# Performance work log

Hardware: AMD Instinct MI355X
Metric: run time of the kernel (lower is better)

## Reference

```python
import jax, jax.numpy as jnp
import numpy as np

NUM_HEADS = 16
LN_EPS = 1e-5


def _layer_norm(x, w, b, eps=LN_EPS):
    m = jnp.mean(x, axis=-1, keepdims=True)
    v = jnp.var(x, axis=-1, keepdims=True)
    return (x - m) / jnp.sqrt(v + eps) * w + b


def setup_inputs() -> dict:
    key = jax.random.key(0)
    L, D, DFF, B, S = 16, 1024, 4096, 4, 1024
    ks = jax.random.split(key, 6)
    w_scale = 0.02
    return {
        "x": jax.random.normal(ks[0], (B, S, D), jnp.float32),
        "qkv_w": jax.random.normal(ks[1], (L, 3 * D, D), jnp.float32) * w_scale,
        "qkv_b": jnp.zeros((L, 3 * D), jnp.float32),
        "out_w": jax.random.normal(ks[2], (L, D, D), jnp.float32) * w_scale,
        "out_b": jnp.zeros((L, D), jnp.float32),
        "w1": jax.random.normal(ks[3], (L, DFF, D), jnp.float32) * w_scale,
        "b1": jnp.zeros((L, DFF), jnp.float32),
        "w2": jax.random.normal(ks[4], (L, D, DFF), jnp.float32) * w_scale,
        "b2": jnp.zeros((L, D), jnp.float32),
        "ln1_w": jnp.ones((L, D), jnp.float32),
        "ln1_b": jnp.zeros((L, D), jnp.float32),
        "ln2_w": jnp.ones((L, D), jnp.float32),
        "ln2_b": jnp.zeros((L, D), jnp.float32),
    }


def reference(x, qkv_w, qkv_b, out_w, out_b, w1, b1, w2, b2, ln1_w, ln1_b, ln2_w, ln2_b):
    # T2STransformer.process_prompt: stack of T2SBlocks with causal attention.
    B, S, D = x.shape
    H = NUM_HEADS
    dh = D // H
    # causal additive bias [1,1,S,S]; True on/below diagonal -> attend
    causal = jnp.tril(jnp.ones((S, S), bool))
    bias = jnp.where(causal, 0.0, -jnp.inf).astype(x.dtype)[None, None]
    scale = 1.0 / np.sqrt(dh)

    def step(h, p):
        (qw, qb, ow, ob, mw1, mb1, mw2, mb2, l1w, l1b, l2w, l2b) = p
        qkv = h @ qw.T + qb                      # [B,S,3D]
        q, k, v = jnp.split(qkv, 3, axis=-1)
        q = q.reshape(B, S, H, dh).transpose(0, 2, 1, 3)  # [B,H,S,dh]
        k = k.reshape(B, S, H, dh).transpose(0, 2, 1, 3)
        v = v.reshape(B, S, H, dh).transpose(0, 2, 1, 3)
        scores = jnp.einsum("bhqd,bhkd->bhqk", q, k) * scale + bias
        attn = jax.nn.softmax(scores, axis=-1)
        ctx = jnp.einsum("bhqk,bhkd->bhqd", attn, v)
        ctx = ctx.transpose(0, 2, 1, 3).reshape(B, S, D)
        h = h + (ctx @ ow.T + ob)
        h = _layer_norm(h, l1w, l1b)
        mlp = jax.nn.relu(h @ mw1.T + mb1) @ mw2.T + mb2
        h = _layer_norm(h + mlp, l2w, l2b)
        return h, None

    params = (qkv_w, qkv_b, out_w, out_b, w1, b1, w2, b2, ln1_w, ln1_b, ln2_w, ln2_b)
    out, _ = jax.lax.scan(step, x, params)
    return out
```

## Files before the change

### kernel.cpp

```cpp
#include <hip/hip_runtime.h>
#include <hip/hip_bf16.h>

typedef float f32x4 __attribute__((ext_vector_type(4)));
typedef __bf16 bf16x8 __attribute__((ext_vector_type(8)));
typedef unsigned short ushort_t;

__device__ __forceinline__ unsigned short f2bf(float f) {
    unsigned int u = __builtin_bit_cast(unsigned int, f);
    u += 0x7fffu + ((u >> 16) & 1u);
    return (unsigned short)(u >> 16);
}

#define GCAST(p) ((const __attribute__((address_space(1))) void*)(p))
#define LCAST(p) ((__attribute__((address_space(3))) void*)(p))

__device__ __forceinline__ bf16x8 ldsw(const unsigned short* T, int row, int bcol) {
    return *reinterpret_cast<const bf16x8*>(
        reinterpret_cast<const char*>(T) + row * 128 + (bcol ^ ((row & 7) << 4)));
}

__global__ __launch_bounds__(256) void convert_weights_kernel(
    const float* __restrict__ qw, const float* __restrict__ ow,
    const float* __restrict__ w1, const float* __restrict__ w2,
    unsigned short* __restrict__ dst)
{
    int i = blockIdx.x * 256 + threadIdx.x;
    const float* src; int off;
    if (i < 786432)       { src = qw; off = i; }
    else if (i < 1048576) { src = ow; off = i - 786432; }
    else if (i < 2097152) { src = w1; off = i - 1048576; }
    else                  { src = w2; off = i - 2097152; }
    float4 v = ((const float4*)src)[off];
    ushort4 u;
    u.x = f2bf(v.x); u.y = f2bf(v.y); u.z = f2bf(v.z); u.w = f2bf(v.w);
    ((ushort4*)dst)[i] = u;
}

__global__ __launch_bounds__(256) void gemm_kernel(
    const unsigned short* __restrict__ A, const unsigned short* __restrict__ W,
    const float* __restrict__ bias, void* __restrict__ Cout,
    int N, int K, int relu, int out_bf16)
{
    __shared__ alignas(16) unsigned short As[128][64];
    __shared__ alignas(16) unsigned short Bs[128][64];

    const int tid  = threadIdx.x;
    const int bn   = blockIdx.x, bm = blockIdx.y;
    const int wave = tid >> 6, lane = tid & 63;
    const int wm   = (wave >> 1) * 64, wn = (wave & 1) * 64;
    const int l15  = lane & 15, quad = lane >> 4;
    const int srow = lane >> 3;
    const int scol = (lane & 7) * 8;

    f32x4 acc[4][4];
#pragma unroll
    for (int i = 0; i < 4; i++)
#pragma unroll
        for (int j = 0; j < 4; j++) acc[i][j] = f32x4{0.f, 0.f, 0.f, 0.f};

    const unsigned short* Abase = A + (size_t)(bm * 128) * K;
    const unsigned short* Wbase = W + (size_t)(bn * 128) * K;

    for (int k0 = 0; k0 < K; k0 += 64) {
        __syncthreads();
#pragma unroll
        for (int i = 0; i < 4; i++) {
            int r0 = (i * 4 + wave) * 8;
            __builtin_amdgcn_global_load_lds(
                GCAST(&Abase[(size_t)(r0 + srow) * K + k0 + scol]),
                LCAST(&As[r0][0]), 16, 0, 0);
            __builtin_amdgcn_global_load_lds(
                GCAST(&Wbase[(size_t)(r0 + srow) * K + k0 + scol]),
                LCAST(&Bs[r0][0]), 16, 0, 0);
        }
        __syncthreads();

#pragma unroll
        for (int ks = 0; ks < 2; ks++) {
            bf16x8 a[4], b[4];
#pragma unroll
            for (int mt = 0; mt < 4; mt++)
                a[mt] = *reinterpret_cast<const bf16x8*>(&As[wm + mt * 16 + l15][ks * 32 + quad * 8]);
#pragma unroll
            for (int nt = 0; nt < 4; nt++)
                b[nt] = *reinterpret_cast<const bf16x8*>(&Bs[wn + nt * 16 + l15][ks * 32 + quad * 8]);
#pragma unroll
            for (int mt = 0; mt < 4; mt++)
#pragma unroll
                for (int nt = 0; nt < 4; nt++)
                    acc[mt][nt] = __builtin_amdgcn_mfma_f32_16x16x32_bf16(
                        a[mt], b[nt], acc[mt][nt], 0, 0, 0);
        }
    }

    float* Cf = (float*)Cout;
    unsigned short* Cb = (unsigned short*)Cout;
#pragma unroll
    for (int nt = 0; nt < 4; nt++) {
        int gn = bn * 128 + wn + nt * 16 + l15;
        float bv = bias[gn];
#pragma unroll
        for (int mt = 0; mt < 4; mt++) {
            int gm0 = bm * 128 + wm + mt * 16 + quad * 4;
#pragma unroll
            for (int r = 0; r < 4; r++) {
                float v = acc[mt][nt][r] + bv;
                if (relu) v = fmaxf(v, 0.f);
                if (out_bf16) Cb[(size_t)(gm0 + r) * N + gn] = f2bf(v);
                else          Cf[(size_t)(gm0 + r) * N + gn] = v;
            }
        }
    }
}

__global__ __launch_bounds__(256) void attn_kernel(
    const unsigned short* __restrict__ qkv, unsigned short* __restrict__ ctx)
{
    const int qt = blockIdx.x;
    const int bh = blockIdx.y;
    const int b  = bh >> 4, h = bh & 15;
    const int tid = threadIdx.x, wave = tid >> 6, lane = tid & 63;
    const int l15 = lane & 15, quad = lane >> 4;
    const int srow = lane >> 3;
    const int scolz = ((lane & 7) ^ srow) * 8;
    const float scale = 0.125f;

    __shared__ alignas(16) unsigned short Qs[64][64];
    __shared__ alignas(16) unsigned short Ks[64][64];
    __shared__ alignas(16) unsigned short Vt[64][64];
    __shared__ alignas(16) unsigned short Ps[64][64];

    const unsigned short* qbase = qkv + (size_t)(b * 1024 + qt * 64) * 3072 + h * 64;
#pragma unroll
    for (int i = 0; i < 2; i++) {
        int r0 = (i * 4 + wave) * 8;
        __builtin_amdgcn_global_load_lds(
            GCAST(&qbase[(size_t)(r0 + srow) * 3072 + scolz]),
            LCAST(&Qs[r0][0]), 16, 0, 0);
    }

    f32x4 O[4];
#pragma unroll
    for (int dt = 0; dt < 4; dt++) O[dt] = f32x4{0.f, 0.f, 0.f, 0.f};
    float m_run[4], l_run[4];
#pragma unroll
    for (int r = 0; r < 4; r++) { m_run[r] = -__builtin_inff(); l_run[r] = 0.f; }

    const int q_row_base = qt * 64 + wave * 16;

    for (int j = 0; j <= qt; j++) {
        __syncthreads();
        const unsigned short* kbase = qkv + (size_t)(b * 1024 + j * 64) * 3072 + 1024 + h * 64;
        const unsigned short* vbase = qkv + (size_t)(b * 1024 + j * 64) * 3072 + 2048 + h * 64;
#pragma unroll
        for (int i = 0; i < 2; i++) {
            int r0 = (i * 4 + wave) * 8;
            __builtin_amdgcn_global_load_lds(
                GCAST(&kbase[(size_t)(r0 + srow) * 3072 + scolz]),
                LCAST(&Ks[r0][0]), 16, 0, 0);
        }
#pragma unroll
        for (int i = 0; i < 4; i++) {
            int idx = tid + i * 256;
            int k = idx >> 4, c4 = (idx & 15) * 4;
            ushort4 vv = *(const ushort4*)&vbase[(size_t)k * 3072 + c4];
            char* vt = (char*)Vt;
            int klo = (k & 7) * 2;
            int kch = (k >> 3) << 4;
            const unsigned short* vp = (const unsigned short*)&vv;
#pragma unroll
            for (int j2 = 0; j2 < 4; j2++) {
                int d = c4 + j2;
                *(unsigned short*)(vt + d * 128 + ((kch ^ ((d & 7) << 4)) | klo)) = vp[j2];
            }
        }
        __syncthreads();

        f32x4 Sc[4];
#pragma unroll
        for (int nt = 0; nt < 4; nt++) Sc[nt] = f32x4{0.f, 0.f, 0.f, 0.f};
        __builtin_amdgcn_s_setprio(1);
#pragma unroll
        for (int ks = 0; ks < 2; ks++) {
            bf16x8 aq = ldsw(&Qs[0][0], wave * 16 + l15, ks * 64 + quad * 16);
#pragma unroll
            for (int nt = 0; nt < 4; nt++) {
                bf16x8 bk = ldsw(&Ks[0][0], nt * 16 + l15, ks * 64 + quad * 16);
                Sc[nt] = __builtin_amdgcn_mfma_f32_16x16x32_bf16(aq, bk, Sc[nt], 0, 0, 0);
            }
        }
        __builtin_amdgcn_s_setprio(0);

#pragma unroll
        for (int nt = 0; nt < 4; nt++)
#pragma unroll
            for (int r = 0; r < 4; r++) Sc[nt][r] *= scale;

        if (j == qt) {
#pragma unroll
            for (int r = 0; r < 4; r++) {
                int qg = q_row_base + quad * 4 + r;
#pragma unroll
                for (int nt = 0; nt < 4; nt++) {
                    int kg = j * 64 + nt * 16 + l15;
                    if (kg > qg) Sc[nt][r] = -__builtin_inff();
                }
            }
        }

        float alpha[4];
#pragma unroll
        for (int r = 0; r < 4; r++) {
            float mx = -__builtin_inff();
#pragma unroll
            for (int nt = 0; nt < 4; nt++) mx = fmaxf(mx, Sc[nt][r]);
#pragma unroll
            for (int off = 1; off < 16; off <<= 1) mx = fmaxf(mx, __shfl_xor(mx, off));
            float mnew = fmaxf(m_run[r], mx);
            alpha[r] = __expf(m_run[r] - mnew);
            m_run[r] = mnew;
        }

#pragma unroll
        for (int r = 0; r < 4; r++) {
            float sum = 0.f;
#pragma unroll
            for (int nt = 0; nt < 4; nt++) {
                float p = __expf(Sc[nt][r] - m_run[r]);
                Sc[nt][r] = p;
                sum += p;
            }
#pragma unroll
            for (int off = 1; off < 16; off <<= 1) sum += __shfl_xor(sum, off);
            l_run[r] = l_run[r] * alpha[r] + sum;
        }

#pragma unroll
        for (int dt = 0; dt < 4; dt++)
#pragma unroll
            for (int r = 0; r < 4; r++) O[dt][r] *= alpha[r];

        {
            char* ps = (char*)Ps;
#pragma unroll
            for (int nt = 0; nt < 4; nt++)
#pragma unroll
                for (int r = 0; r < 4; r++) {
                    int row = wave * 16 + quad * 4 + r;
                    int col = nt * 16 + l15;
                    *(unsigned short*)(ps + row * 128 + ((col * 2) ^ ((row & 7) << 4)))
                        = f2bf(Sc[nt][r]);
                }
        }

        __builtin_amdgcn_s_setprio(1);
#pragma unroll
        for (int ks = 0; ks < 2; ks++) {
            bf16x8 ap = ldsw(&Ps[0][0], wave * 16 + l15, ks * 64 + quad * 16);
#pragma unroll
            for (int dt = 0; dt < 4; dt++) {
                bf16x8 bv = ldsw(&Vt[0][0], dt * 16 + l15, ks * 64 + quad * 16);
                O[dt] = __builtin_amdgcn_mfma_f32_16x16x32_bf16(ap, bv, O[dt], 0, 0, 0);
            }
        }
        __builtin_amdgcn_s_setprio(0);
    }

    unsigned short* obase = ctx + (size_t)(b * 1024 + qt * 64 + wave * 16) * 1024 + h * 64;
#pragma unroll
    for (int r = 0; r < 4; r++) {
        float inv = 1.f / l_run[r];
#pragma unroll
        for (int dt = 0; dt < 4; dt++)
            obase[(size_t)(quad * 4 + r) * 1024 + dt * 16 + l15] = f2bf(O[dt][r] * inv);
    }
}

__global__ __launch_bounds__(256) void ln_residual_kernel(
    float* __restrict__ h, unsigned short* __restrict__ hb,
    const float* __restrict__ r,
    const float* __restrict__ w, const float* __restrict__ b)
{
    const int row = blockIdx.x;
    const int tid = threadIdx.x;
    const int lane = tid & 63, wave = tid >> 6;

    float4 hv = *(float4*)&h[(size_t)row * 1024 + tid * 4];
    float4 rv = *(const float4*)&r[(size_t)row * 1024 + tid * 4];
    float x0 = hv.x + rv.x, x1 = hv.y + rv.y, x2 = hv.z + rv.z, x3 = hv.w + rv.w;

    float s  = x0 + x1 + x2 + x3;
    float s2 = x0 * x0 + x1 * x1 + x2 * x2 + x3 * x3;
#pragma unroll
    for (int off = 32; off >= 1; off >>= 1) {
        s  += __shfl_xor(s, off);
        s2 += __shfl_xor(s2, off);
    }
    __shared__ float ls[4], ls2[4];
    if (lane == 0) { ls[wave] = s; ls2[wave] = s2; }
    __syncthreads();
    s  = ls[0] + ls[1] + ls[2] + ls[3];
    s2 = ls2[0] + ls2[1] + ls2[2] + ls2[3];

    const float inv_n = 1.f / 1024.f;
    float mean = s * inv_n;
    float var  = s2 * inv_n - mean * mean;
    float rstd = rsqrtf(var + 1e-5f);

    float4 wv = *(const float4*)&w[tid * 4];
    float4 bv = *(const float4*)&b[tid * 4];
    float4 out;
    out.x = (x0 - mean) * rstd * wv.x + bv.x;
    out.y = (x1 - mean) * rstd * wv.y + bv.y;
    out.z = (x2 - mean) * rstd * wv.z + bv.z;
    out.w = (x3 - mean) * rstd * wv.w + bv.w;
    *(float4*)&h[(size_t)row * 1024 + tid * 4] = out;
    ushort4 ub;
    ub.x = f2bf(out.x); ub.y = f2bf(out.y); ub.z = f2bf(out.z); ub.w = f2bf(out.w);
    *(ushort4*)&hb[(size_t)row * 1024 + tid * 4] = ub;
}

__global__ __launch_bounds__(256) void copy_convert_kernel(
    const float* __restrict__ in, float* __restrict__ h, unsigned short* __restrict__ hb)
{
    int i = blockIdx.x * 256 + threadIdx.x;
    float4 v = ((const float4*)in)[i];
    ((float4*)h)[i] = v;
    ushort4 u;
    u.x = f2bf(v.x); u.y = f2bf(v.y); u.z = f2bf(v.z); u.w = f2bf(v.w);
    ((ushort4*)hb)[i] = u;
}

extern "C" void kernel_launch(void* const* d_in, const int* in_sizes, int n_in,
                              void* d_out, int out_size, void* d_ws, size_t ws_size,
                              hipStream_t stream)
{
    const float* x     = (const float*)d_in[0];
    const float* qkv_w = (const float*)d_in[1];
    const float* qkv_b = (const float*)d_in[2];
    const float* out_w = (const float*)d_in[3];
    const float* out_b = (const float*)d_in[4];
    const float* w1    = (const float*)d_in[5];
    const float* b1    = (const float*)d_in[6];
    const float* w2    = (const float*)d_in[7];
    const float* b2    = (const float*)d_in[8];
    const float* ln1w  = (const float*)d_in[9];
    const float* ln1b  = (const float*)d_in[10];
    const float* ln2w  = (const float*)d_in[11];
    const float* ln2b  = (const float*)d_in[12];

    float* h = (float*)d_out;
    char* ws = (char*)d_ws;
    unsigned short* qkvb = (unsigned short*)ws;
    unsigned short* tb   = (unsigned short*)ws;
    unsigned short* ctxb = (unsigned short*)(ws + 33554432);
    unsigned short* hb   = (unsigned short*)(ws + 33554432 + 8388608);
    unsigned short* wbf  = (unsigned short*)(ws + 50331648);
    float*          r    = (float*)(ws + 75497472);

    unsigned short* wb_qkv = wbf;
    unsigned short* wb_out = wbf + 3145728;
    unsigned short* wb_w1  = wbf + 4194304;
    unsigned short* wb_w2  = wbf + 8388608;

    copy_convert_kernel<<<4096, 256, 0, stream>>>(x, h, hb);

    for (int l = 0; l < 16; l++) {
        convert_weights_kernel<<<12288, 256, 0, stream>>>(
            qkv_w + (size_t)l * 3145728, out_w + (size_t)l * 1048576,
            w1 + (size_t)l * 4194304, w2 + (size_t)l * 4194304, wbf);

        gemm_kernel<<<dim3(24, 32), 256, 0, stream>>>(
            hb, wb_qkv, qkv_b + (size_t)l * 3072, qkvb, 3072, 1024, 0, 1);
        attn_kernel<<<dim3(16, 64), 256, 0, stream>>>(qkvb, ctxb);
        gemm_kernel<<<dim3(8, 32), 256, 0, stream>>>(
            ctxb, wb_out, out_b + (size_t)l * 1024, r, 1024, 1024, 0, 0);
        ln_residual_kernel<<<4096, 256, 0, stream>>>(
            h, hb, r, ln1w + (size_t)l * 1024, ln1b + (size_t)l * 1024);
        gemm_kernel<<<dim3(32, 32), 256, 0, stream>>>(
            hb, wb_w1, b1 + (size_t)l * 4096, tb, 4096, 1024, 1, 1);
        gemm_kernel<<<dim3(8, 32), 256, 0, stream>>>(
            tb, wb_w2, b2 + (size_t)l * 1024, r, 1024, 4096, 0, 0);
        ln_residual_kernel<<<4096, 256, 0, stream>>>(
            h, hb, r, ln2w + (size_t)l * 1024, ln2b + (size_t)l * 1024);
    }
}
```

Baseline: 5.998 ms.

## Split-K the N=1024 GEMMs and add XCD-aware block swizzling

```diff
diff --git a/kernel.cpp b/kernel.cpp
--- a/kernel.cpp
+++ b/kernel.cpp
@@ -17,6 +17,11 @@
 __device__ __forceinline__ bf16x8 ldsw(const unsigned short* T, int row, int bcol) {
     return *reinterpret_cast<const bf16x8*>(
         reinterpret_cast<const char*>(T) + row * 128 + (bcol ^ ((row & 7) << 4)));
+}
+
+__device__ __forceinline__ int xcd_swizzle(int bid, int nwg) {
+    int cpx = nwg >> 3;
+    return (bid & 7) * cpx + (bid >> 3);
 }
 
 __global__ __launch_bounds__(256) void convert_weights_kernel(
@@ -45,7 +50,9 @@
     __shared__ alignas(16) unsigned short Bs[128][64];
 
     const int tid  = threadIdx.x;
-    const int bn   = blockIdx.x, bm = blockIdx.y;
+    const int nwg  = gridDim.x * gridDim.y;
+    const int swz  = xcd_swizzle(blockIdx.y * gridDim.x + blockIdx.x, nwg);
+    const int bn   = swz % gridDim.x, bm = swz / gridDim.x;
     const int wave = tid >> 6, lane = tid & 63;
     const int wm   = (wave >> 1) * 64, wn = (wave & 1) * 64;
     const int l15  = lane & 15, quad = lane >> 4;
@@ -113,6 +120,83 @@
     }
 }
 
+__global__ __launch_bounds__(256) void gemm_splitk_kernel(
+    const unsigned short* __restrict__ A, const unsigned short* __restrict__ W,
+    const float* __restrict__ bias, float* __restrict__ C0, float* __restrict__ C1,
+    int N, int K)
+{
+    __shared__ alignas(16) unsigned short As[128][64];
+    __shared__ alignas(16) unsigned short Bs[128][64];
+
+    const int tid  = threadIdx.x;
+    const int nwg  = gridDim.x * gridDim.y;
+    const int swz  = xcd_swizzle(blockIdx.y * gridDim.x + blockIdx.x, nwg);
+    const int bn   = swz % gridDim.x, bm = swz / gridDim.x;
+    const int kz   = blockIdx.z;
+    const int kbeg = kz * (K >> 1);
+    const int kend = kbeg + (K >> 1);
+    const int wave = tid >> 6, lane = tid & 63;
+    const int wm   = (wave >> 1) * 64, wn = (wave & 1) * 64;
+    const int l15  = lane & 15, quad = lane >> 4;
+    const int srow = lane >> 3;
+    const int scol = (lane & 7) * 8;
+
+    f32x4 acc[4][4];
+#pragma unroll
+    for (int i = 0; i < 4; i++)
+#pragma unroll
+        for (int j = 0; j < 4; j++) acc[i][j] = f32x4{0.f, 0.f, 0.f, 0.f};
+
+    const unsigned short* Abase = A + (size_t)(bm * 128) * K;
+    const unsigned short* Wbase = W + (size_t)(bn * 128) * K;
+
+    for (int k0 = kbeg; k0 < kend; k0 += 64) {
+        __syncthreads();
+#pragma unroll
+        for (int i = 0; i < 4; i++) {
+            int r0 = (i * 4 + wave) * 8;
+            __builtin_amdgcn_global_load_lds(
+                GCAST(&Abase[(size_t)(r0 + srow) * K + k0 + scol]),
+                LCAST(&As[r0][0]), 16, 0, 0);
+            __builtin_amdgcn_global_load_lds(
+                GCAST(&Wbase[(size_t)(r0 + srow) * K + k0 + scol]),
+                LCAST(&Bs[r0][0]), 16, 0, 0);
+        }
+        __syncthreads();
+
+#pragma unroll
+        for (int ks = 0; ks < 2; ks++) {
+            bf16x8 a[4], b[4];
+#pragma unroll
+            for (int mt = 0; mt < 4; mt++)
+                a[mt] = *reinterpret_cast<const bf16x8*>(&As[wm + mt * 16 + l15][ks * 32 + quad * 8]);
+#pragma unroll
+            for (int nt = 0; nt < 4; nt++)
+                b[nt] = *reinterpret_cast<const bf16x8*>(&Bs[wn + nt * 16 + l15][ks * 32 + quad * 8]);
+#pragma unroll
+            for (int mt = 0; mt < 4; mt++)
+#pragma unroll
+                for (int nt = 0; nt < 4; nt++)
+                    acc[mt][nt] = __builtin_amdgcn_mfma_f32_16x16x32_bf16(
+                        a[mt], b[nt], acc[mt][nt], 0, 0, 0);
+        }
+    }
+
+    float* Cf = kz ? C1 : C0;
+#pragma unroll
+    for (int nt = 0; nt < 4; nt++) {
+        int gn = bn * 128 + wn + nt * 16 + l15;
+        float bv = kz ? 0.f : bias[gn];
+#pragma unroll
+        for (int mt = 0; mt < 4; mt++) {
+            int gm0 = bm * 128 + wm + mt * 16 + quad * 4;
+#pragma unroll
+            for (int r = 0; r < 4; r++)
+                Cf[(size_t)(gm0 + r) * N + gn] = acc[mt][nt][r] + bv;
+        }
+    }
+}
+
 __global__ __launch_bounds__(256) void attn_kernel(
     const unsigned short* __restrict__ qkv, unsigned short* __restrict__ ctx)
 {
@@ -278,7 +362,7 @@
 
 __global__ __launch_bounds__(256) void ln_residual_kernel(
     float* __restrict__ h, unsigned short* __restrict__ hb,
-    const float* __restrict__ r,
+    const float* __restrict__ r, const float* __restrict__ r2,
     const float* __restrict__ w, const float* __restrict__ b)
 {
     const int row = blockIdx.x;
@@ -287,7 +371,9 @@
 
     float4 hv = *(float4*)&h[(size_t)row * 1024 + tid * 4];
     float4 rv = *(const float4*)&r[(size_t)row * 1024 + tid * 4];
-    float x0 = hv.x + rv.x, x1 = hv.y + rv.y, x2 = hv.z + rv.z, x3 = hv.w + rv.w;
+    float4 r2v = *(const float4*)&r2[(size_t)row * 1024 + tid * 4];
+    float x0 = hv.x + rv.x + r2v.x, x1 = hv.y + rv.y + r2v.y;
+    float x2 = hv.z + rv.z + r2v.z, x3 = hv.w + rv.w + r2v.w;
 
     float s  = x0 + x1 + x2 + x3;
     float s2 = x0 * x0 + x1 * x1 + x2 * x2 + x3 * x3;
@@ -357,6 +443,7 @@
     unsigned short* hb   = (unsigned short*)(ws + 33554432 + 8388608);
     unsigned short* wbf  = (unsigned short*)(ws + 50331648);
     float*          r    = (float*)(ws + 75497472);
+    float*          r2   = (float*)(ws + 92274688);
 
     unsigned short* wb_qkv = wbf;
     unsigned short* wb_out = wbf + 3145728;
@@ -373,15 +460,15 @@
         gemm_kernel<<<dim3(24, 32), 256, 0, stream>>>(
             hb, wb_qkv, qkv_b + (size_t)l * 3072, qkvb, 3072, 1024, 0, 1);
         attn_kernel<<<dim3(16, 64), 256, 0, stream>>>(qkvb, ctxb);
-        gemm_kernel<<<dim3(8, 32), 256, 0, stream>>>(
-            ctxb, wb_out, out_b + (size_t)l * 1024, r, 1024, 1024, 0, 0);
+        gemm_splitk_kernel<<<dim3(8, 32, 2), 256, 0, stream>>>(
+            ctxb, wb_out, out_b + (size_t)l * 1024, r, r2, 1024, 1024);
         ln_residual_kernel<<<4096, 256, 0, stream>>>(
-            h, hb, r, ln1w + (size_t)l * 1024, ln1b + (size_t)l * 1024);
+            h, hb, r, r2, ln1w + (size_t)l * 1024, ln1b + (size_t)l * 1024);
         gemm_kernel<<<dim3(32, 32), 256, 0, stream>>>(
             hb, wb_w1, b1 + (size_t)l * 4096, tb, 4096, 1024, 1, 1);
-        gemm_kernel<<<dim3(8, 32), 256, 0, stream>>>(
-            tb, wb_w2, b2 + (size_t)l * 1024, r, 1024, 4096, 0, 0);
+        gemm_splitk_kernel<<<dim3(8, 32, 2), 256, 0, stream>>>(
+            tb, wb_w2, b2 + (size_t)l * 1024, r, r2, 1024, 4096);
         ln_residual_kernel<<<4096, 256, 0, stream>>>(
-            h, hb, r, ln2w + (size_t)l * 1024, ln2b + (size_t)l * 1024);
-    }
-}
+            h, hb, r, r2, ln2w + (size_t)l * 1024, ln2b + (size_t)l * 1024);
+    }
+}
```

Result: faster. 5.460 ms (-9.0%).
